# Kernel tuning notes

Measured on AMD Instinct MI355X. Metric: run time of the kernel, lower is better.

## Reference

```python
import jax, jax.numpy as jnp
import numpy as np

N = 50000
E = 800000
NHID = 128
NOUT = 64
NLAYER = 4
BN_EPS = 1e-5


def setup_inputs() -> dict:
    key = jax.random.key(0)
    ks = jax.random.split(key, 4)
    x = jax.random.normal(ks[0], (N, NHID), dtype=jnp.float32)
    edge_index = jax.random.randint(ks[1], (2, E), 0, N, dtype=jnp.int32)
    Ws = jax.random.normal(ks[2], (NLAYER, NHID, NHID), dtype=jnp.float32) / np.sqrt(NHID)
    bs = jnp.zeros((NLAYER, NHID), dtype=jnp.float32)
    gammas = jnp.ones((NLAYER, NHID), dtype=jnp.float32)
    betas = jnp.zeros((NLAYER, NHID), dtype=jnp.float32)
    Wout = jax.random.normal(ks[3], (NHID, NOUT), dtype=jnp.float32) / np.sqrt(NHID)
    bout = jnp.zeros((NOUT,), dtype=jnp.float32)
    return {"x": x, "edge_index": edge_index, "Ws": Ws, "bs": bs,
            "gammas": gammas, "betas": betas, "Wout": Wout, "bout": bout}


def _gcn_conv(x, src, dst, norm, W, b):
    # GCNConv: h = x W, then symmetric-normalized scatter-add over edges (+ self loops already in src/dst)
    h = x @ W                                   # [N, nhid]
    msgs = h[src] * norm[:, None]               # [E+N, nhid] gather + scale
    agg = jax.ops.segment_sum(msgs, dst, num_segments=N)  # scatter-add
    return agg + b


def _batchnorm(x, gamma, beta):
    mean = jnp.mean(x, axis=0)
    var = jnp.mean(jnp.square(x - mean), axis=0)  # biased var (torch BN)
    return (x - mean) * jax.lax.rsqrt(var + BN_EPS) * gamma + beta


def reference(x, edge_index, Ws, bs, gammas, betas, Wout, bout):
    # add self loops
    loops = jnp.arange(N, dtype=edge_index.dtype)
    src = jnp.concatenate([edge_index[0], loops])
    dst = jnp.concatenate([edge_index[1], loops])
    # symmetric degree normalization: deg^-1/2[src] * deg^-1/2[dst]
    deg = jax.ops.segment_sum(jnp.ones_like(dst, dtype=x.dtype), dst, num_segments=N)
    dinv = jax.lax.rsqrt(jnp.maximum(deg, 1.0))
    norm = dinv[src] * dinv[dst]

    prev = x
    for l in range(NLAYER):
        h = _gcn_conv(x, src, dst, norm, Ws[l], bs[l])
        h = _batchnorm(h, gammas[l], betas[l])
        h = jax.nn.relu(h)
        # dropout p=0.0 -> identity
        x = h + prev  # residual
        prev = x
    return x @ Wout + bout
```

## Files before the change

kernel.cpp:

```cpp
#include <hip/hip_runtime.h>

#define NN 50000
#define NE 800000
#define NH 128
#define NO 64
#define NL 4
#define BN_EPS 1e-5f
#define NB1 ((NN + 255) / 256)
#define NGB (NN / 8)

typedef __attribute__((ext_vector_type(8))) short short8;
typedef __attribute__((ext_vector_type(4))) float f32x4;
typedef __attribute__((ext_vector_type(4))) unsigned int u32x4;

__device__ inline unsigned short f2bf(float f) {
    unsigned int u = __float_as_uint(f);
    return (unsigned short)((u + 0x7fffu + ((u >> 16) & 1u)) >> 16);
}
__device__ inline float bflo(unsigned int u) { return __uint_as_float(u << 16); }
__device__ inline float bfhi(unsigned int u) { return __uint_as_float(u & 0xffff0000u); }
__device__ inline unsigned pk(float a, float b) {
    return (unsigned)f2bf(a) | ((unsigned)f2bf(b) << 16);
}

__global__ void k_degrank(const int* __restrict__ dst, int* __restrict__ deg_r,
                          int* __restrict__ rank) {
    int base = (blockIdx.x * 256 + threadIdx.x) * 2;
    if (base >= NE) return;
    int2 d2 = *(const int2*)&dst[base];
    int r0 = (base >> 9) & 3;
    int2 rr;
    rr.x = atomicAdd(&deg_r[r0 * NN + d2.x], 1);
    rr.y = atomicAdd(&deg_r[r0 * NN + d2.y], 1);
    *(int2*)&rank[base] = rr;
}

__global__ void k_scan1(const int* __restrict__ deg_r, int* __restrict__ off,
                        int* __restrict__ aux, float* __restrict__ dinv,
                        int* __restrict__ degT, int* __restrict__ offR) {
    __shared__ int ls[256];
    int i = blockIdx.x * 256 + threadIdx.x;
    int c0 = 0, c1 = 0, c2 = 0, c3 = 0;
    if (i < NN) {
        c0 = deg_r[i]; c1 = deg_r[NN + i];
        c2 = deg_r[2 * NN + i]; c3 = deg_r[3 * NN + i];
    }
    int v = c0 + c1 + c2 + c3;
    ls[threadIdx.x] = v;
    __syncthreads();
    for (int s = 1; s < 256; s <<= 1) {
        int t = (threadIdx.x >= s) ? ls[threadIdx.x - s] : 0;
        __syncthreads();
        ls[threadIdx.x] += t;
        __syncthreads();
    }
    if (i < NN) {
        off[i] = ls[threadIdx.x] - v;
        dinv[i] = rsqrtf((float)v + 1.0f);
        degT[i] = v;
        offR[i] = 0;
        offR[NN + i] = c0;
        offR[2 * NN + i] = c0 + c1;
        offR[3 * NN + i] = c0 + c1 + c2;
    }
    if (threadIdx.x == 255) aux[blockIdx.x] = ls[255];
}

__global__ void k_scan2(int* __restrict__ aux) {
    __shared__ int ls[256];
    int v = (threadIdx.x < NB1) ? aux[threadIdx.x] : 0;
    ls[threadIdx.x] = v;
    __syncthreads();
    for (int s = 1; s < 256; s <<= 1) {
        int t = (threadIdx.x >= s) ? ls[threadIdx.x - s] : 0;
        __syncthreads();
        ls[threadIdx.x] += t;
        __syncthreads();
    }
    if (threadIdx.x < NB1) aux[threadIdx.x] = ls[threadIdx.x] - v;
}

__global__ void k_fill(const int* __restrict__ src, const int* __restrict__ dst,
                       const int* __restrict__ off, const int* __restrict__ aux,
                       const int* __restrict__ offR, const int* __restrict__ rank,
                       int* __restrict__ csr) {
    int base = (blockIdx.x * 256 + threadIdx.x) * 4;
    if (base >= NE) return;
    int4 d4 = *(const int4*)&dst[base];
    int4 r4 = *(const int4*)&rank[base];
    int4 s4 = *(const int4*)&src[base];
    const int* oR = offR + ((base >> 9) & 3) * NN;
    csr[off[d4.x] + aux[d4.x >> 8] + oR[d4.x] + r4.x] = s4.x;
    csr[off[d4.y] + aux[d4.y >> 8] + oR[d4.y] + r4.y] = s4.y;
    csr[off[d4.z] + aux[d4.z >> 8] + oR[d4.z] + r4.z] = s4.z;
    csr[off[d4.w] + aux[d4.w >> 8] + oR[d4.w] + r4.w] = s4.w;
}

__global__ void k_pack(const float* __restrict__ Ws, const float* __restrict__ Wout,
                       unsigned short* __restrict__ Wpk, unsigned short* __restrict__ Wopk) {
    int t = blockIdx.x * 256 + threadIdx.x;
    if (t < NL * 16384) {
        int l = t >> 14, r = t & 16383;
        int ks = r >> 12, ct = (r >> 9) & 7, lane = (r >> 3) & 63, i = r & 7;
        int k = ks * 32 + (lane >> 4) * 8 + i;
        int n = ct * 16 + (lane & 15);
        Wpk[t] = f2bf(Ws[l * 16384 + k * 128 + n]);
    } else if (t < NL * 16384 + 8192) {
        int r = t - NL * 16384;
        int ks = r >> 11, ct = (r >> 9) & 3, lane = (r >> 3) & 63, i = r & 7;
        int k = ks * 32 + (lane >> 4) * 8 + i;
        int n = ct * 16 + (lane & 15);
        Wopk[r] = f2bf(Wout[k * 64 + n]);
    }
}

__global__ __launch_bounds__(256) void k_fg0(const float* __restrict__ X,
                                             const unsigned short* __restrict__ Wpk,
                                             const float* __restrict__ dinv,
                                             unsigned short* __restrict__ Hd) {
    int w = threadIdx.x >> 6, l = threadIdx.x & 63;
    int row0 = blockIdx.x * 64 + w * 16;
    int lo = l & 15, hi = l >> 4;
    int arow = row0 + lo;
    int crow = (arow < NN) ? arow : NN - 1;
    short8 frag[4];
#pragma unroll
    for (int g = 0; g < 4; g++) {
        int cs = g * 32 + hi * 8;
        float4 p0 = *(const float4*)&X[(size_t)crow * NH + cs];
        float4 p1 = *(const float4*)&X[(size_t)crow * NH + cs + 4];
        short8 f;
        f[0] = (short)f2bf(p0.x); f[1] = (short)f2bf(p0.y);
        f[2] = (short)f2bf(p0.z); f[3] = (short)f2bf(p0.w);
        f[4] = (short)f2bf(p1.x); f[5] = (short)f2bf(p1.y);
        f[6] = (short)f2bf(p1.z); f[7] = (short)f2bf(p1.w);
        frag[g] = f;
    }
    const short8* Wv = (const short8*)Wpk;
    int srow = row0 + hi * 4;
    float dv[4];
#pragma unroll
    for (int r = 0; r < 4; r++) dv[r] = (srow + r < NN) ? dinv[srow + r] : 0.0f;
#pragma unroll
    for (int ct = 0; ct < 8; ct++) {
        f32x4 acc = {0.0f, 0.0f, 0.0f, 0.0f};
#pragma unroll
        for (int g = 0; g < 4; g++)
            acc = __builtin_amdgcn_mfma_f32_16x16x32_bf16(frag[g], Wv[(g * 8 + ct) * 64 + l], acc, 0, 0, 0);
        int col = ct * 16 + lo;
#pragma unroll
        for (int r = 0; r < 4; r++) {
            int grow = srow + r;
            if (grow < NN) Hd[grow * NH + col] = f2bf(acc[r] * dv[r]);
        }
    }
}

__global__ __launch_bounds__(256) void k_fg(const unsigned short* __restrict__ AGGb,
                                            const float* __restrict__ scale,
                                            const float* __restrict__ shift,
                                            const float* __restrict__ Xprev,
                                            float* __restrict__ Xout,
                                            const unsigned short* __restrict__ Wpk,
                                            const float* __restrict__ dinv,
                                            unsigned short* __restrict__ Hd) {
    int w = threadIdx.x >> 6, l = threadIdx.x & 63;
    int row0 = blockIdx.x * 64 + w * 16;
    int lo = l & 15, hi = l >> 4;
    int arow = row0 + lo;
    bool valid = arow < NN;
    int crow = valid ? arow : NN - 1;
    short8 frag[4];
#pragma unroll
    for (int g = 0; g < 4; g++) {
        int cs = g * 32 + hi * 8;
        uint4 ab = *(const uint4*)&AGGb[(size_t)crow * NH + cs];
        float4 p0 = *(const float4*)&Xprev[(size_t)crow * NH + cs];
        float4 p1 = *(const float4*)&Xprev[(size_t)crow * NH + cs + 4];
        float4 sc0 = *(const float4*)&scale[cs];
        float4 sc1 = *(const float4*)&scale[cs + 4];
        float4 sh0 = *(const float4*)&shift[cs];
        float4 sh1 = *(const float4*)&shift[cs + 4];
        float o0 = fmaxf(fmaf(bflo(ab.x), sc0.x, sh0.x), 0.0f) + p0.x;
        float o1 = fmaxf(fmaf(bfhi(ab.x), sc0.y, sh0.y), 0.0f) + p0.y;
        float o2 = fmaxf(fmaf(bflo(ab.y), sc0.z, sh0.z), 0.0f) + p0.z;
        float o3 = fmaxf(fmaf(bfhi(ab.y), sc0.w, sh0.w), 0.0f) + p0.w;
        float o4 = fmaxf(fmaf(bflo(ab.z), sc1.x, sh1.x), 0.0f) + p1.x;
        float o5 = fmaxf(fmaf(bfhi(ab.z), sc1.y, sh1.y), 0.0f) + p1.y;
        float o6 = fmaxf(fmaf(bflo(ab.w), sc1.z, sh1.z), 0.0f) + p1.z;
        float o7 = fmaxf(fmaf(bfhi(ab.w), sc1.w, sh1.w), 0.0f) + p1.w;
        if (valid) {
            float4 s0 = {o0, o1, o2, o3}, s1 = {o4, o5, o6, o7};
            *(float4*)&Xout[(size_t)arow * NH + cs] = s0;
            *(float4*)&Xout[(size_t)arow * NH + cs + 4] = s1;
        }
        short8 f;
        f[0] = (short)f2bf(o0); f[1] = (short)f2bf(o1);
        f[2] = (short)f2bf(o2); f[3] = (short)f2bf(o3);
        f[4] = (short)f2bf(o4); f[5] = (short)f2bf(o5);
        f[6] = (short)f2bf(o6); f[7] = (short)f2bf(o7);
        frag[g] = f;
    }
    const short8* Wv = (const short8*)Wpk;
    int srow = row0 + hi * 4;
    float dv[4];
#pragma unroll
    for (int r = 0; r < 4; r++) dv[r] = (srow + r < NN) ? dinv[srow + r] : 0.0f;
#pragma unroll
    for (int ct = 0; ct < 8; ct++) {
        f32x4 acc = {0.0f, 0.0f, 0.0f, 0.0f};
#pragma unroll
        for (int g = 0; g < 4; g++)
            acc = __builtin_amdgcn_mfma_f32_16x16x32_bf16(frag[g], Wv[(g * 8 + ct) * 64 + l], acc, 0, 0, 0);
        int col = ct * 16 + lo;
#pragma unroll
        for (int r = 0; r < 4; r++) {
            int grow = srow + r;
            if (grow < NN) Hd[grow * NH + col] = f2bf(acc[r] * dv[r]);
        }
    }
}

__global__ __launch_bounds__(256) void k_fgout(const unsigned short* __restrict__ AGGb,
                                               const float* __restrict__ scale,
                                               const float* __restrict__ shift,
                                               const float* __restrict__ Xprev,
                                               const unsigned short* __restrict__ Wpk,
                                               const float* __restrict__ b,
                                               float* __restrict__ out) {
    int w = threadIdx.x >> 6, l = threadIdx.x & 63;
    int row0 = blockIdx.x * 64 + w * 16;
    int lo = l & 15, hi = l >> 4;
    int arow = row0 + lo;
    int crow = (arow < NN) ? arow : NN - 1;
    short8 frag[4];
#pragma unroll
    for (int g = 0; g < 4; g++) {
        int cs = g * 32 + hi * 8;
        uint4 ab = *(const uint4*)&AGGb[(size_t)crow * NH + cs];
        float4 p0 = *(const float4*)&Xprev[(size_t)crow * NH + cs];
        float4 p1 = *(const float4*)&Xprev[(size_t)crow * NH + cs + 4];
        float4 sc0 = *(const float4*)&scale[cs];
        float4 sc1 = *(const float4*)&scale[cs + 4];
        float4 sh0 = *(const float4*)&shift[cs];
        float4 sh1 = *(const float4*)&shift[cs + 4];
        short8 f;
        f[0] = (short)f2bf(fmaxf(fmaf(bflo(ab.x), sc0.x, sh0.x), 0.0f) + p0.x);
        f[1] = (short)f2bf(fmaxf(fmaf(bfhi(ab.x), sc0.y, sh0.y), 0.0f) + p0.y);
        f[2] = (short)f2bf(fmaxf(fmaf(bflo(ab.y), sc0.z, sh0.z), 0.0f) + p0.z);
        f[3] = (short)f2bf(fmaxf(fmaf(bfhi(ab.y), sc0.w, sh0.w), 0.0f) + p0.w);
        f[4] = (short)f2bf(fmaxf(fmaf(bflo(ab.z), sc1.x, sh1.x), 0.0f) + p1.x);
        f[5] = (short)f2bf(fmaxf(fmaf(bfhi(ab.z), sc1.y, sh1.y), 0.0f) + p1.y);
        f[6] = (short)f2bf(fmaxf(fmaf(bflo(ab.w), sc1.z, sh1.z), 0.0f) + p1.z);
        f[7] = (short)f2bf(fmaxf(fmaf(bfhi(ab.w), sc1.w, sh1.w), 0.0f) + p1.w);
        frag[g] = f;
    }
    const short8* Wv = (const short8*)Wpk;
    int srow = row0 + hi * 4;
#pragma unroll
    for (int ct = 0; ct < 4; ct++) {
        f32x4 acc = {0.0f, 0.0f, 0.0f, 0.0f};
#pragma unroll
        for (int g = 0; g < 4; g++)
            acc = __builtin_amdgcn_mfma_f32_16x16x32_bf16(frag[g], Wv[(g * 4 + ct) * 64 + l], acc, 0, 0, 0);
        int col = ct * 16 + lo;
        float bb = b[col];
#pragma unroll
        for (int r = 0; r < 4; r++) {
            int grow = srow + r;
            if (grow < NN) out[grow * NO + col] = acc[r] + bb;
        }
    }
}

__global__ __launch_bounds__(256) void k_gather(const unsigned short* __restrict__ Hd,
                                                const int* __restrict__ csr,
                                                const int* __restrict__ off,
                                                const int* __restrict__ aux,
                                                const int* __restrict__ degT,
                                                const float* __restrict__ dinv,
                                                unsigned short* __restrict__ AGGb,
                                                float* __restrict__ partial) {
    int b = blockIdx.x;
    int slot = threadIdx.x >> 5;
    int half = (threadIdx.x >> 4) & 1;
    int q = threadIdx.x & 15;
    int g = b * 8 + slot;
    const u32x4* Hv = (const u32x4*)Hd;
    int o = off[g] + aux[g >> 8];
    int d = degT[g];
    float a0 = 0, a1 = 0, a2 = 0, a3 = 0, a4 = 0, a5 = 0, a6 = 0, a7 = 0;
    if (!half) {
        u32x4 h = Hv[g * 16 + q];
        a0 = bflo(h.x); a1 = bfhi(h.x);
        a2 = bflo(h.y); a3 = bfhi(h.y);
        a4 = bflo(h.z); a5 = bfhi(h.z);
        a6 = bflo(h.w); a7 = bfhi(h.w);
    }
    int dh = d >> 1;
    int j = half ? dh : 0;
    int je = half ? d : dh;
    for (; j + 4 <= je; j += 4) {
        int s0 = __builtin_nontemporal_load(&csr[o + j]);
        int s1 = __builtin_nontemporal_load(&csr[o + j + 1]);
        int s2 = __builtin_nontemporal_load(&csr[o + j + 2]);
        int s3 = __builtin_nontemporal_load(&csr[o + j + 3]);
        u32x4 h0 = Hv[s0 * 16 + q];
        u32x4 h1 = Hv[s1 * 16 + q];
        u32x4 h2 = Hv[s2 * 16 + q];
        u32x4 h3 = Hv[s3 * 16 + q];
        a0 += (bflo(h0.x) + bflo(h1.x)) + (bflo(h2.x) + bflo(h3.x));
        a1 += (bfhi(h0.x) + bfhi(h1.x)) + (bfhi(h2.x) + bfhi(h3.x));
        a2 += (bflo(h0.y) + bflo(h1.y)) + (bflo(h2.y) + bflo(h3.y));
        a3 += (bfhi(h0.y) + bfhi(h1.y)) + (bfhi(h2.y) + bfhi(h3.y));
        a4 += (bflo(h0.z) + bflo(h1.z)) + (bflo(h2.z) + bflo(h3.z));
        a5 += (bfhi(h0.z) + bfhi(h1.z)) + (bfhi(h2.z) + bfhi(h3.z));
        a6 += (bflo(h0.w) + bflo(h1.w)) + (bflo(h2.w) + bflo(h3.w));
        a7 += (bfhi(h0.w) + bfhi(h1.w)) + (bfhi(h2.w) + bfhi(h3.w));
    }
    for (; j < je; j++) {
        int s0 = __builtin_nontemporal_load(&csr[o + j]);
        u32x4 h0 = Hv[s0 * 16 + q];
        a0 += bflo(h0.x); a1 += bfhi(h0.x);
        a2 += bflo(h0.y); a3 += bfhi(h0.y);
        a4 += bflo(h0.z); a5 += bfhi(h0.z);
        a6 += bflo(h0.w); a7 += bfhi(h0.w);
    }
    a0 += __shfl_xor(a0, 16); a1 += __shfl_xor(a1, 16);
    a2 += __shfl_xor(a2, 16); a3 += __shfl_xor(a3, 16);
    a4 += __shfl_xor(a4, 16); a5 += __shfl_xor(a5, 16);
    a6 += __shfl_xor(a6, 16); a7 += __shfl_xor(a7, 16);
    float dv = dinv[g];
    a0 *= dv; a1 *= dv; a2 *= dv; a3 *= dv;
    a4 *= dv; a5 *= dv; a6 *= dv; a7 *= dv;
    if (!half) {
        u32x4 u;
        u.x = pk(a0, a1); u.y = pk(a2, a3);
        u.z = pk(a4, a5); u.w = pk(a6, a7);
        __builtin_nontemporal_store(u, &((u32x4*)AGGb)[g * 16 + q]);
    }
    float t0 = a0 * a0, t1 = a1 * a1, t2 = a2 * a2, t3 = a3 * a3;
    float t4 = a4 * a4, t5 = a5 * a5, t6 = a6 * a6, t7 = a7 * a7;
#define RED(v) v += __shfl_xor(v, 32);
    RED(a0) RED(a1) RED(a2) RED(a3) RED(a4) RED(a5) RED(a6) RED(a7)
    RED(t0) RED(t1) RED(t2) RED(t3) RED(t4) RED(t5) RED(t6) RED(t7)
#undef RED
    __shared__ float ws[4][16][16];
    int wv = threadIdx.x >> 6, lane = threadIdx.x & 63;
    if (lane < 16) {
        ws[wv][lane][0] = a0; ws[wv][lane][1] = a1;
        ws[wv][lane][2] = a2; ws[wv][lane][3] = a3;
        ws[wv][lane][4] = a4; ws[wv][lane][5] = a5;
        ws[wv][lane][6] = a6; ws[wv][lane][7] = a7;
        ws[wv][lane][8] = t0; ws[wv][lane][9] = t1;
        ws[wv][lane][10] = t2; ws[wv][lane][11] = t3;
        ws[wv][lane][12] = t4; ws[wv][lane][13] = t5;
        ws[wv][lane][14] = t6; ws[wv][lane][15] = t7;
    }
    __syncthreads();
    if (threadIdx.x < 16) {
        int qq = threadIdx.x;
#pragma unroll
        for (int k = 0; k < 8; k++) {
            float sv = ws[0][qq][k] + ws[1][qq][k] + ws[2][qq][k] + ws[3][qq][k];
            float qv = ws[0][qq][k + 8] + ws[1][qq][k + 8] + ws[2][qq][k + 8] + ws[3][qq][k + 8];
            __builtin_nontemporal_store(sv, &partial[(size_t)b * 256 + qq * 8 + k]);
            __builtin_nontemporal_store(qv, &partial[(size_t)b * 256 + 128 + qq * 8 + k]);
        }
    }
}

__global__ __launch_bounds__(256) void k_statred(const float* __restrict__ partial,
                                                 const float* __restrict__ gamma,
                                                 const float* __restrict__ beta,
                                                 float* __restrict__ scale,
                                                 float* __restrict__ shift) {
    int s = blockIdx.x;
    int t = threadIdx.x;
    float sum = 0.0f, sq = 0.0f;
    for (int k = t; k < NGB; k += 256) {
        sum += partial[(size_t)k * 256 + s];
        sq  += partial[(size_t)k * 256 + 128 + s];
    }
    __shared__ float ls[256], lq[256];
    ls[t] = sum; lq[t] = sq;
    __syncthreads();
    for (int st = 128; st > 0; st >>= 1) {
        if (t < st) { ls[t] += ls[t + st]; lq[t] += lq[t + st]; }
        __syncthreads();
    }
    if (t == 0) {
        float mean = ls[0] * (1.0f / NN);
        float var = lq[0] * (1.0f / NN) - mean * mean;
        float istd = rsqrtf(var + BN_EPS);
        float sc = istd * gamma[s];
        scale[s] = sc;
        shift[s] = beta[s] - mean * sc;
    }
}

extern "C" void kernel_launch(void* const* d_in, const int* in_sizes, int n_in,
                              void* d_out, int out_size, void* d_ws, size_t ws_size,
                              hipStream_t stream) {
    const float* x    = (const float*)d_in[0];
    const int*   ei   = (const int*)d_in[1];
    const float* Ws   = (const float*)d_in[2];
    const float* gam  = (const float*)d_in[4];
    const float* bet  = (const float*)d_in[5];
    const float* Wout = (const float*)d_in[6];
    const float* bout = (const float*)d_in[7];
    float* out = (float*)d_out;

    const int* src = ei;
    const int* dst = ei + NE;

    char* p = (char*)d_ws;
    auto alloc = [&](size_t bytes) { char* r = p; p += (bytes + 255) & ~(size_t)255; return r; };
    int*   deg_r = (int*)alloc((size_t)4 * NN * 4);
    int*   offR  = (int*)alloc((size_t)4 * NN * 4);
    int*   degT  = (int*)alloc(NN * 4);
    int*   off   = (int*)alloc(NN * 4);
    int*   rank  = (int*)alloc((size_t)NE * 4);
    int*   aux   = (int*)alloc(256 * 4);
    int*   csr   = (int*)alloc((size_t)NE * 4);
    float* dinv  = (float*)alloc(NN * 4);
    float* XA    = (float*)alloc((size_t)NN * NH * 4);
    float* XB    = (float*)alloc((size_t)NN * NH * 4);
    unsigned short* Hd   = (unsigned short*)alloc((size_t)NN * NH * 2);
    unsigned short* AGGb = (unsigned short*)alloc((size_t)NN * NH * 2);
    unsigned short* Wpk  = (unsigned short*)alloc((size_t)NL * NH * NH * 2);
    unsigned short* Wopk = (unsigned short*)alloc((size_t)NH * NO * 2);
    float* partial = (float*)alloc((size_t)NGB * 256 * 4);
    float* scale = (float*)alloc(NH * 4);
    float* shift = (float*)alloc(NH * 4);

    hipMemsetAsync(deg_r, 0, (size_t)4 * NN * 4, stream);
    k_degrank<<<(NE / 2 + 255) / 256, 256, 0, stream>>>(dst, deg_r, rank);
    k_scan1<<<NB1, 256, 0, stream>>>(deg_r, off, aux, dinv, degT, offR);
    k_scan2<<<1, 256, 0, stream>>>(aux);
    k_fill<<<(NE / 4 + 255) / 256, 256, 0, stream>>>(src, dst, off, aux, offR, rank, csr);
    k_pack<<<(NL * 16384 + 8192 + 255) / 256, 256, 0, stream>>>(Ws, Wout, Wpk, Wopk);

    const int GB = (NN + 63) / 64;

    k_fg0<<<GB, 256, 0, stream>>>(x, Wpk, dinv, Hd);

    const float* xprev = x;
    for (int l = 0; l < NL; l++) {
        k_gather<<<NGB, 256, 0, stream>>>(Hd, csr, off, aux, degT, dinv, AGGb, partial);
        k_statred<<<128, 256, 0, stream>>>(partial, gam + l * NH, bet + l * NH, scale, shift);
        if (l < NL - 1) {
            float* Xout = (l & 1) ? XB : XA;
            k_fg<<<GB, 256, 0, stream>>>(AGGb, scale, shift, xprev, Xout,
                                         Wpk + (size_t)(l + 1) * 16384, dinv, Hd);
            xprev = Xout;
        } else {
            k_fgout<<<GB, 256, 0, stream>>>(AGGb, scale, shift, xprev, Wopk, bout, out);
        }
    }
}
```

Measured before the change: 396.1 us.

## Assign one 16-lane group per node in gather, dropping split-degree halves

The gather kernel now processes 16 destination nodes per 256-thread block with one 16-lane group per node, instead of 8 nodes with each node's edge list split between two 16-lane halves. This removes the half-combine shuffle and the masked store. It also halves the number of blocks and partial-stat rows, which shrinks the statistics reduction. Nontemporal loads and stores are replaced with ordinary accesses. In exchange, each lane walks the full neighbour list serially, which lowers memory-level parallelism per node and may lengthen the tail for high-degree nodes.

```diff
diff --git a/kernel.cpp b/kernel.cpp
--- a/kernel.cpp
+++ b/kernel.cpp
@@ -7,11 +7,10 @@
 #define NL 4
 #define BN_EPS 1e-5f
 #define NB1 ((NN + 255) / 256)
-#define NGB (NN / 8)
+#define NGB (NN / 16)
 
 typedef __attribute__((ext_vector_type(8))) short short8;
 typedef __attribute__((ext_vector_type(4))) float f32x4;
-typedef __attribute__((ext_vector_type(4))) unsigned int u32x4;
 
 __device__ inline unsigned short f2bf(float f) {
     unsigned int u = __float_as_uint(f);
@@ -282,33 +281,24 @@
                                                 unsigned short* __restrict__ AGGb,
                                                 float* __restrict__ partial) {
     int b = blockIdx.x;
-    int slot = threadIdx.x >> 5;
-    int half = (threadIdx.x >> 4) & 1;
-    int q = threadIdx.x & 15;
-    int g = b * 8 + slot;
-    const u32x4* Hv = (const u32x4*)Hd;
+    int slot = threadIdx.x >> 4, q = threadIdx.x & 15;
+    int g = b * 16 + slot;
+    const uint4* Hv = (const uint4*)Hd;
     int o = off[g] + aux[g >> 8];
     int d = degT[g];
-    float a0 = 0, a1 = 0, a2 = 0, a3 = 0, a4 = 0, a5 = 0, a6 = 0, a7 = 0;
-    if (!half) {
-        u32x4 h = Hv[g * 16 + q];
-        a0 = bflo(h.x); a1 = bfhi(h.x);
-        a2 = bflo(h.y); a3 = bfhi(h.y);
-        a4 = bflo(h.z); a5 = bfhi(h.z);
-        a6 = bflo(h.w); a7 = bfhi(h.w);
-    }
-    int dh = d >> 1;
-    int j = half ? dh : 0;
-    int je = half ? d : dh;
-    for (; j + 4 <= je; j += 4) {
-        int s0 = __builtin_nontemporal_load(&csr[o + j]);
-        int s1 = __builtin_nontemporal_load(&csr[o + j + 1]);
-        int s2 = __builtin_nontemporal_load(&csr[o + j + 2]);
-        int s3 = __builtin_nontemporal_load(&csr[o + j + 3]);
-        u32x4 h0 = Hv[s0 * 16 + q];
-        u32x4 h1 = Hv[s1 * 16 + q];
-        u32x4 h2 = Hv[s2 * 16 + q];
-        u32x4 h3 = Hv[s3 * 16 + q];
+    uint4 h = Hv[g * 16 + q];
+    float a0 = bflo(h.x), a1 = bfhi(h.x);
+    float a2 = bflo(h.y), a3 = bfhi(h.y);
+    float a4 = bflo(h.z), a5 = bfhi(h.z);
+    float a6 = bflo(h.w), a7 = bfhi(h.w);
+    int j = 0;
+    for (; j + 4 <= d; j += 4) {
+        int s0 = csr[o + j], s1 = csr[o + j + 1];
+        int s2 = csr[o + j + 2], s3 = csr[o + j + 3];
+        uint4 h0 = Hv[s0 * 16 + q];
+        uint4 h1 = Hv[s1 * 16 + q];
+        uint4 h2 = Hv[s2 * 16 + q];
+        uint4 h3 = Hv[s3 * 16 + q];
         a0 += (bflo(h0.x) + bflo(h1.x)) + (bflo(h2.x) + bflo(h3.x));
         a1 += (bfhi(h0.x) + bfhi(h1.x)) + (bfhi(h2.x) + bfhi(h3.x));
         a2 += (bflo(h0.y) + bflo(h1.y)) + (bflo(h2.y) + bflo(h3.y));
@@ -318,30 +308,24 @@
         a6 += (bflo(h0.w) + bflo(h1.w)) + (bflo(h2.w) + bflo(h3.w));
         a7 += (bfhi(h0.w) + bfhi(h1.w)) + (bfhi(h2.w) + bfhi(h3.w));
     }
-    for (; j < je; j++) {
-        int s0 = __builtin_nontemporal_load(&csr[o + j]);
-        u32x4 h0 = Hv[s0 * 16 + q];
+    for (; j < d; j++) {
+        int s0 = csr[o + j];
+        uint4 h0 = Hv[s0 * 16 + q];
         a0 += bflo(h0.x); a1 += bfhi(h0.x);
         a2 += bflo(h0.y); a3 += bfhi(h0.y);
         a4 += bflo(h0.z); a5 += bfhi(h0.z);
         a6 += bflo(h0.w); a7 += bfhi(h0.w);
     }
-    a0 += __shfl_xor(a0, 16); a1 += __shfl_xor(a1, 16);
-    a2 += __shfl_xor(a2, 16); a3 += __shfl_xor(a3, 16);
-    a4 += __shfl_xor(a4, 16); a5 += __shfl_xor(a5, 16);
-    a6 += __shfl_xor(a6, 16); a7 += __shfl_xor(a7, 16);
     float dv = dinv[g];
     a0 *= dv; a1 *= dv; a2 *= dv; a3 *= dv;
     a4 *= dv; a5 *= dv; a6 *= dv; a7 *= dv;
-    if (!half) {
-        u32x4 u;
-        u.x = pk(a0, a1); u.y = pk(a2, a3);
-        u.z = pk(a4, a5); u.w = pk(a6, a7);
-        __builtin_nontemporal_store(u, &((u32x4*)AGGb)[g * 16 + q]);
-    }
+    uint4 u;
+    u.x = pk(a0, a1); u.y = pk(a2, a3);
+    u.z = pk(a4, a5); u.w = pk(a6, a7);
+    ((uint4*)AGGb)[g * 16 + q] = u;
     float t0 = a0 * a0, t1 = a1 * a1, t2 = a2 * a2, t3 = a3 * a3;
     float t4 = a4 * a4, t5 = a5 * a5, t6 = a6 * a6, t7 = a7 * a7;
-#define RED(v) v += __shfl_xor(v, 32);
+#define RED(v) v += __shfl_xor(v, 16); v += __shfl_xor(v, 32);
     RED(a0) RED(a1) RED(a2) RED(a3) RED(a4) RED(a5) RED(a6) RED(a7)
     RED(t0) RED(t1) RED(t2) RED(t3) RED(t4) RED(t5) RED(t6) RED(t7)
 #undef RED
@@ -364,8 +348,8 @@
         for (int k = 0; k < 8; k++) {
             float sv = ws[0][qq][k] + ws[1][qq][k] + ws[2][qq][k] + ws[3][qq][k];
             float qv = ws[0][qq][k + 8] + ws[1][qq][k + 8] + ws[2][qq][k + 8] + ws[3][qq][k + 8];
-            __builtin_nontemporal_store(sv, &partial[(size_t)b * 256 + qq * 8 + k]);
-            __builtin_nontemporal_store(qv, &partial[(size_t)b * 256 + 128 + qq * 8 + k]);
+            partial[(size_t)b * 256 + qq * 8 + k] = sv;
+            partial[(size_t)b * 256 + 128 + qq * 8 + k] = qv;
         }
     }
 }
```

New measurement: 322.4 us. 1.23x faster.
